# Optimization experiments

Hardware: AMD Instinct MI355X
Metric: run time of the kernel (lower is better)

## Reference

```python
import jax, jax.numpy as jnp
import numpy as np

S, P, T, E, H = 32, 48, 8, 64, 64      # scenes, peds/scene, obs_len, embedding_dim, h_dim
D1, D2 = 512, 1024                      # mlp_pre_pool hidden / bottleneck dims
B = S * P
TOTAL_LEN = 20                          # obs_len + pred_len (8 + 12)


def setup_inputs() -> dict:
    key = jax.random.key(0)
    ks = jax.random.split(key, 10)
    h_states = jax.random.normal(ks[0], (1, B, H), jnp.float32)
    end_pos = jax.random.normal(ks[1], (B, 2), jnp.float32)
    traj = jax.random.normal(ks[2], (TOTAL_LEN, B, 2), jnp.float32)
    traj_weight = jax.random.uniform(ks[3], (S, P * P, 2, T), jnp.float32)
    starts = jnp.arange(S, dtype=jnp.int32) * P
    seq_start_end = jnp.stack([starts, starts + P], axis=1)  # uniform scenes of P peds
    # learned params
    W_se = jax.random.normal(ks[4], (T * E, 2 * T), jnp.float32) * 0.05  # spatial_embedding
    b_se = jnp.zeros((T * E,), jnp.float32)
    W1 = jax.random.normal(ks[5], (D1, T * E + H), jnp.float32) * 0.05   # 576 -> 512
    b1 = jnp.zeros((D1,), jnp.float32)
    W2 = jax.random.normal(ks[6], (D2, D1), jnp.float32) * 0.05          # 512 -> 1024
    b2 = jnp.zeros((D2,), jnp.float32)
    return {"h_states": h_states, "seq_start_end": seq_start_end, "end_pos": end_pos,
            "traj": traj, "traj_weight": traj_weight, "mlp_pre_pool_dim_0": T * E,
            "W_se": W_se, "b_se": b_se, "W1": W1, "b1": b1, "W2": W2, "b2": b2}


def reference(h_states, seq_start_end, end_pos, traj, traj_weight, mlp_pre_pool_dim_0,
              W_se, b_se, W1, b1, W2, b2):
    # obs_traj: (obs_len, B, 2) -> (B, T, 2) -> per-scene (S, P, T, 2)
    obs = traj[:T].transpose(1, 0, 2).reshape(S, P, T, 2)
    h = h_states.reshape(S, P, H)
    # pairwise history differences: row (i, j) = obs[j] - obs[i]  (gather-diff)
    rel = obs[:, None, :, :, :] - obs[:, :, None, :, :]          # (S, i, j, T, 2)
    rel = rel.reshape(S, P, P, 2 * T)                            # flatten (T,2) -> 2T
    emb = rel @ W_se.T + b_se                                    # (S, P, P, T*E)
    # traj_weight[i]: (P*P, 2, T) -> permute(0,2,1) -> tile channel to E -> flatten
    w = jnp.transpose(traj_weight, (0, 1, 3, 2))                 # (S, P*P, T, 2)
    w = jnp.tile(w, (1, 1, 1, E // 2)).reshape(S, P, P, T * E)
    emb = w * emb
    # curr_hidden_1: hidden of ped j broadcast over i
    hj = jnp.broadcast_to(h[:, None, :, :], (S, P, P, H))
    x = jnp.concatenate([emb, hj], axis=-1)                      # (S, P, P, 576)
    x = jax.nn.relu(x @ W1.T + b1)                               # (S, P, P, 512)
    x = jax.nn.relu(x @ W2.T + b2)                               # (S, P, P, 1024)
    pool_h = x.max(axis=2)                                       # max over j
    return pool_h.reshape(S * P, D2)
```

## Files before the change

kernel.cpp:

```cpp
#include <hip/hip_runtime.h>
#include <hip/hip_bf16.h>
#include <stdint.h>

#define S_  32
#define P_  48
#define T_  8
#define E_  64
#define H_  64
#define D1_ 512
#define D2_ 1024
#define B_  (S_*P_)
#define M_  (S_*P_*P_)
#define K1_ 576
#define KE_ 512

typedef __attribute__((ext_vector_type(8))) short  short8;
typedef __attribute__((ext_vector_type(8))) __bf16 bf16x8;
typedef __attribute__((ext_vector_type(4))) float  f32x4;
typedef __attribute__((ext_vector_type(8))) float  f32x8;

__device__ inline short f2bf(float x) {
  union { float f; unsigned u; } v; v.f = x;
  unsigned r = v.u + 0x7FFFu + ((v.u >> 16) & 1u);
  return (short)(r >> 16);
}

__device__ inline void async16(const void* g, void* l) {
  __builtin_amdgcn_global_load_lds(
      (const __attribute__((address_space(1))) void*)g,
      (__attribute__((address_space(3))) void*)l, 16, 0, 0);
}

__device__ inline f32x4 mfma16(short8 a, short8 b, f32x4 c) {
  return __builtin_amdgcn_mfma_f32_16x16x32_bf16(
      __builtin_bit_cast(bf16x8, a), __builtin_bit_cast(bf16x8, b), c, 0, 0, 0);
}

__global__ __launch_bounds__(256) void k_cvt_w(const float* __restrict__ W1,
                                               const float* __restrict__ W2,
                                               short* __restrict__ W1b,
                                               short* __restrict__ W2b) {
  int idx = blockIdx.x * 256 + threadIdx.x;
  if (idx < D1_ * K1_) W1b[idx] = f2bf(W1[idx]);
  int idx2 = idx - D1_ * K1_;
  if (idx2 >= 0 && idx2 < D2_ * D1_) W2b[idx2] = f2bf(W2[idx2]);
}

__global__ __launch_bounds__(256) void k_oW(const float* __restrict__ traj,
                                            const float* __restrict__ Wse,
                                            float* __restrict__ oW) {
  int bid = blockIdx.x;
  int p = bid >> 1;
  int n = ((bid & 1) << 8) + threadIdx.x;
  float obs[16];
#pragma unroll
  for (int t = 0; t < T_; ++t) {
    obs[2*t]   = traj[(t*B_ + p)*2 + 0];
    obs[2*t+1] = traj[(t*B_ + p)*2 + 1];
  }
  float acc = 0.f;
#pragma unroll
  for (int k = 0; k < 16; ++k) acc += obs[k] * Wse[n*16 + k];
  oW[p*KE_ + n] = acc;
}

__global__ __launch_bounds__(256) void k_build_x(const float* __restrict__ tw,
                                                 const float* __restrict__ h,
                                                 const float* __restrict__ bse,
                                                 const float* __restrict__ oW,
                                                 short* __restrict__ X) {
  int tid = threadIdx.x;
  int wid = tid >> 6, lane = tid & 63;
  int row = blockIdx.x * 4 + wid;
  int s   = row / (P_ * P_);
  int rem = row - s * (P_ * P_);
  int i   = rem / P_;
  int j   = rem - i * P_;
  int bi = s * P_ + i, bj = s * P_ + j;

  const float* twq = tw + (size_t)(s * (P_*P_) + rem) * 16;
  int t = lane >> 3;
  float w0 = twq[t];
  float w1 = twq[8 + t];

  int n0 = lane * 8;
  f32x8 vj = *(const f32x8*)&oW[(size_t)bj * KE_ + n0];
  f32x8 vi = *(const f32x8*)&oW[(size_t)bi * KE_ + n0];
  f32x8 vb = *(const f32x8*)&bse[n0];
  short8 o;
#pragma unroll
  for (int k = 0; k < 8; ++k) {
    float e = (vj[k] - vi[k] + vb[k]) * ((k & 1) ? w1 : w0);
    o[k] = f2bf(e);
  }
  *(short8*)&X[(size_t)row * K1_ + n0] = o;

  if (lane < 8) {
    f32x8 vh = *(const f32x8*)&h[(size_t)bj * H_ + lane * 8];
    short8 oh;
#pragma unroll
    for (int k = 0; k < 8; ++k) oh[k] = f2bf(vh[k]);
    *(short8*)&X[(size_t)row * K1_ + KE_ + lane * 8] = oh;
  }
}

__global__ __launch_bounds__(256) void k_gemm1(const short* __restrict__ X,
                                               const short* __restrict__ W1b,
                                               const float* __restrict__ b1,
                                               short* __restrict__ X1) {
  __shared__ short Ae[128*64], Ao[128*64], Be[128*64], Bo[128*64];
  int tid = threadIdx.x;
  int wid = tid >> 6, lane = tid & 63;
  int wgid = (blockIdx.x & 7) * (2304/8) + (blockIdx.x >> 3);
  int tm = wgid >> 2, tn = wgid & 3;
  int brow = tm * 128, bcol = tn * 128;
  int wr = wid >> 1, wc = wid & 1;
  int lr = lane & 15, lhi = lane >> 4;
  int sx = lr & 7;

  f32x4 acc[4][4];
#pragma unroll
  for (int m = 0; m < 4; ++m)
#pragma unroll
    for (int n = 0; n < 4; ++n) acc[m][n] = (f32x4){0.f, 0.f, 0.f, 0.f};

  auto stage = [&](short* Ab, short* Bb, int k0) {
#pragma unroll
    for (int it = 0; it < 4; ++it) {
      int fg = it * 256 + tid;
      int r = fg >> 3, gs = (fg & 7) ^ (r & 7);
      async16(&X  [(size_t)(brow + r) * K1_ + k0 + (gs << 3)], &Ab[fg * 8]);
    }
#pragma unroll
    for (int it = 0; it < 4; ++it) {
      int fg = it * 256 + tid;
      int r = fg >> 3, gs = (fg & 7) ^ (r & 7);
      async16(&W1b[(size_t)(bcol + r) * K1_ + k0 + (gs << 3)], &Bb[fg * 8]);
    }
  };
  auto compute = [&](const short* Ab, const short* Bb) {
#pragma unroll
    for (int kk = 0; kk < 64; kk += 32) {
      int gr = (kk >> 3) + lhi;
      short8 a[4], b[4];
#pragma unroll
      for (int m = 0; m < 4; ++m)
        a[m] = *(const short8*)&Ab[(wr*64 + m*16 + lr) * 64 + ((gr ^ sx) << 3)];
#pragma unroll
      for (int n = 0; n < 4; ++n)
        b[n] = *(const short8*)&Bb[(wc*64 + n*16 + lr) * 64 + ((gr ^ sx) << 3)];
#pragma unroll
      for (int m = 0; m < 4; ++m)
#pragma unroll
        for (int n = 0; n < 4; ++n)
          acc[m][n] = mfma16(a[m], b[n], acc[m][n]);
    }
  };

  stage(Ae, Be, 0);
  __syncthreads();
  for (int ktp = 0; ktp < 4; ++ktp) {
    stage(Ao, Bo, ktp*128 + 64);
    compute(Ae, Be);
    __syncthreads();
    stage(Ae, Be, ktp*128 + 128);
    compute(Ao, Bo);
    __syncthreads();
  }
  compute(Ae, Be);

#pragma unroll
  for (int n = 0; n < 4; ++n) {
    int gcol = bcol + wc*64 + n*16 + lr;
    float bias = b1[gcol];
#pragma unroll
    for (int m = 0; m < 4; ++m) {
      int grow0 = brow + wr*64 + m*16 + lhi*4;
#pragma unroll
      for (int q = 0; q < 4; ++q) {
        float v = acc[m][n][q] + bias;
        v = v > 0.f ? v : 0.f;
        X1[(size_t)(grow0 + q) * D1_ + gcol] = f2bf(v);
      }
    }
  }
}

__global__ __launch_bounds__(256) void k_gemm2(const short* __restrict__ X1,
                                               const short* __restrict__ W2b,
                                               const float* __restrict__ b2,
                                               float* __restrict__ out) {
  __shared__ short Ae[96*64], Ao[96*64], Be[128*64], Bo[128*64];
  int tid = threadIdx.x;
  int wid = tid >> 6, lane = tid & 63;
  int wgid = (blockIdx.x & 7) * (6144/8) + (blockIdx.x >> 3);
  int tm = wgid >> 3, tn = wgid & 7;
  int brow = tm * 96, bcol = tn * 128;
  int wr = wid >> 1, wc = wid & 1;
  int lr = lane & 15, lhi = lane >> 4;
  int sx = lr & 7;

  f32x4 acc[3][4];
#pragma unroll
  for (int m = 0; m < 3; ++m)
#pragma unroll
    for (int n = 0; n < 4; ++n) acc[m][n] = (f32x4){0.f, 0.f, 0.f, 0.f};

  auto stage = [&](short* Ab, short* Bb, int k0) {
#pragma unroll
    for (int it = 0; it < 3; ++it) {
      int fg = it * 256 + tid;
      int r = fg >> 3, gs = (fg & 7) ^ (r & 7);
      async16(&X1 [(size_t)(brow + r) * D1_ + k0 + (gs << 3)], &Ab[fg * 8]);
    }
#pragma unroll
    for (int it = 0; it < 4; ++it) {
      int fg = it * 256 + tid;
      int r = fg >> 3, gs = (fg & 7) ^ (r & 7);
      async16(&W2b[(size_t)(bcol + r) * D1_ + k0 + (gs << 3)], &Bb[fg * 8]);
    }
  };
  auto compute = [&](const short* Ab, const short* Bb) {
#pragma unroll
    for (int kk = 0; kk < 64; kk += 32) {
      int gr = (kk >> 3) + lhi;
      short8 a[3], b[4];
#pragma unroll
      for (int m = 0; m < 3; ++m)
        a[m] = *(const short8*)&Ab[(wr*48 + m*16 + lr) * 64 + ((gr ^ sx) << 3)];
#pragma unroll
      for (int n = 0; n < 4; ++n)
        b[n] = *(const short8*)&Bb[(wc*64 + n*16 + lr) * 64 + ((gr ^ sx) << 3)];
#pragma unroll
      for (int m = 0; m < 3; ++m)
#pragma unroll
        for (int n = 0; n < 4; ++n)
          acc[m][n] = mfma16(a[m], b[n], acc[m][n]);
    }
  };

  stage(Ae, Be, 0);
  __syncthreads();
  for (int ktp = 0; ktp < 4; ++ktp) {
    stage(Ao, Bo, ktp*128 + 64);
    compute(Ae, Be);
    __syncthreads();
    if (ktp < 3) stage(Ae, Be, ktp*128 + 128);
    compute(Ao, Bo);
    __syncthreads();
  }

  int g = tm * 2 + wr;
#pragma unroll
  for (int n = 0; n < 4; ++n) {
    int gcol = bcol + wc*64 + n*16 + lr;
    float bias = b2[gcol];
    float r = 0.f;
#pragma unroll
    for (int m = 0; m < 3; ++m)
#pragma unroll
      for (int q = 0; q < 4; ++q) {
        float v = acc[m][n][q] + bias;
        if (v > r) r = v;
      }
    r = fmaxf(r, __shfl_xor(r, 16));
    r = fmaxf(r, __shfl_xor(r, 32));
    if (lhi == 0) out[(size_t)g * D2_ + gcol] = r;
  }
}

extern "C" void kernel_launch(void* const* d_in, const int* in_sizes, int n_in,
                              void* d_out, int out_size, void* d_ws, size_t ws_size,
                              hipStream_t stream) {
  const float* h_states = (const float*)d_in[0];
  const float* traj = (const float*)d_in[3];
  const float* tw   = (const float*)d_in[4];
  const float* Wse  = (const float*)d_in[6];
  const float* bse  = (const float*)d_in[7];
  const float* W1   = (const float*)d_in[8];
  const float* b1   = (const float*)d_in[9];
  const float* W2   = (const float*)d_in[10];
  const float* b2   = (const float*)d_in[11];
  float* out = (float*)d_out;

  char* ws = (char*)d_ws;
  const size_t X_BYTES   = (size_t)M_ * K1_ * 2;
  const size_t X1_BYTES  = (size_t)M_ * D1_ * 2;
  const size_t W1B_BYTES = (size_t)D1_ * K1_ * 2;
  short* X   = (short*)ws;
  short* X1  = (short*)(ws + X_BYTES);
  short* W1b = (short*)(ws + X_BYTES + X1_BYTES);
  short* W2b = (short*)(ws + X_BYTES + X1_BYTES + W1B_BYTES);
  float* oW  = (float*)(ws + X_BYTES);

  k_cvt_w  <<<(D1_*K1_ + D2_*D1_ + 255) / 256, 256, 0, stream>>>(W1, W2, W1b, W2b);
  k_oW     <<<B_ * 2, 256, 0, stream>>>(traj, Wse, oW);
  k_build_x<<<M_ / 4, 256, 0, stream>>>(tw, h_states, bse, oW, X);
  k_gemm1  <<<(M_ / 128) * (D1_ / 128), 256, 0, stream>>>(X, W1b, b1, X1);
  k_gemm2  <<<(M_ / 96) * (D2_ / 128), 256, 0, stream>>>(X1, W2b, b2, out);
}
```

Baseline: 255.2 us.

## Enlarge GEMM tiles to 256-wide with 8-wave blocks and MFMA priority hints

Both GEMMs move from 4-wave blocks with 128x128 (gemm1) and 96x128 (gemm2) tiles to 8-wave blocks with 256x256 and 192x256 tiles. Each wave now holds a larger accumulator set, which raises operand reuse per LDS load and cuts global traffic per FLOP. The K loop becomes a single double-buffered loop with explicit vmcnt waits and raw barriers, and MFMA bursts are wrapped in s_setprio. The gemm2 max-pool epilogue now reduces two scene-row groups per wave. The trade-off is fewer blocks (576 and 1536), which may leave CUs underused, plus higher register and LDS pressure that could lower occupancy.

```diff
diff --git a/kernel.cpp b/kernel.cpp
--- a/kernel.cpp
+++ b/kernel.cpp
@@ -104,78 +104,80 @@
   }
 }
 
-__global__ __launch_bounds__(256) void k_gemm1(const short* __restrict__ X,
-                                               const short* __restrict__ W1b,
-                                               const float* __restrict__ b1,
-                                               short* __restrict__ X1) {
-  __shared__ short Ae[128*64], Ao[128*64], Be[128*64], Bo[128*64];
+__global__ __launch_bounds__(512, 2) void k_gemm1(const short* __restrict__ X,
+                                                  const short* __restrict__ W1b,
+                                                  const float* __restrict__ b1,
+                                                  short* __restrict__ X1) {
+  __shared__ short Abuf[2][256 * 64];
+  __shared__ short Bbuf[2][256 * 64];
   int tid = threadIdx.x;
   int wid = tid >> 6, lane = tid & 63;
-  int wgid = (blockIdx.x & 7) * (2304/8) + (blockIdx.x >> 3);
-  int tm = wgid >> 2, tn = wgid & 3;
-  int brow = tm * 128, bcol = tn * 128;
-  int wr = wid >> 1, wc = wid & 1;
+  int wgid = (blockIdx.x & 7) * 72 + (blockIdx.x >> 3);
+  int tm = wgid >> 1, tn = wgid & 1;
+  int brow = tm * 256, bcol = tn * 256;
+  int wr = wid >> 2, wc = wid & 3;
   int lr = lane & 15, lhi = lane >> 4;
   int sx = lr & 7;
 
-  f32x4 acc[4][4];
-#pragma unroll
-  for (int m = 0; m < 4; ++m)
+  f32x4 acc[8][4];
+#pragma unroll
+  for (int m = 0; m < 8; ++m)
 #pragma unroll
     for (int n = 0; n < 4; ++n) acc[m][n] = (f32x4){0.f, 0.f, 0.f, 0.f};
 
-  auto stage = [&](short* Ab, short* Bb, int k0) {
+  auto stage = [&](int buf, int k0) {
 #pragma unroll
     for (int it = 0; it < 4; ++it) {
-      int fg = it * 256 + tid;
+      int fg = it * 512 + tid;
       int r = fg >> 3, gs = (fg & 7) ^ (r & 7);
-      async16(&X  [(size_t)(brow + r) * K1_ + k0 + (gs << 3)], &Ab[fg * 8]);
+      async16(&X  [(size_t)(brow + r) * K1_ + k0 + (gs << 3)], &Abuf[buf][fg * 8]);
     }
 #pragma unroll
     for (int it = 0; it < 4; ++it) {
-      int fg = it * 256 + tid;
+      int fg = it * 512 + tid;
       int r = fg >> 3, gs = (fg & 7) ^ (r & 7);
-      async16(&W1b[(size_t)(bcol + r) * K1_ + k0 + (gs << 3)], &Bb[fg * 8]);
+      async16(&W1b[(size_t)(bcol + r) * K1_ + k0 + (gs << 3)], &Bbuf[buf][fg * 8]);
     }
   };
-  auto compute = [&](const short* Ab, const short* Bb) {
-#pragma unroll
-    for (int kk = 0; kk < 64; kk += 32) {
-      int gr = (kk >> 3) + lhi;
-      short8 a[4], b[4];
-#pragma unroll
-      for (int m = 0; m < 4; ++m)
-        a[m] = *(const short8*)&Ab[(wr*64 + m*16 + lr) * 64 + ((gr ^ sx) << 3)];
+  auto compute = [&](int buf) {
+#pragma unroll
+    for (int kk = 0; kk < 2; ++kk) {
+      int gr = kk * 4 + lhi;
+      short8 a[8], b[4];
+#pragma unroll
+      for (int m = 0; m < 8; ++m)
+        a[m] = *(const short8*)&Abuf[buf][(wr*128 + m*16 + lr) * 64 + ((gr ^ sx) << 3)];
 #pragma unroll
       for (int n = 0; n < 4; ++n)
-        b[n] = *(const short8*)&Bb[(wc*64 + n*16 + lr) * 64 + ((gr ^ sx) << 3)];
-#pragma unroll
-      for (int m = 0; m < 4; ++m)
+        b[n] = *(const short8*)&Bbuf[buf][(wc*64 + n*16 + lr) * 64 + ((gr ^ sx) << 3)];
+      __builtin_amdgcn_s_setprio(1);
+#pragma unroll
+      for (int m = 0; m < 8; ++m)
 #pragma unroll
         for (int n = 0; n < 4; ++n)
           acc[m][n] = mfma16(a[m], b[n], acc[m][n]);
+      __builtin_amdgcn_s_setprio(0);
     }
   };
 
-  stage(Ae, Be, 0);
-  __syncthreads();
-  for (int ktp = 0; ktp < 4; ++ktp) {
-    stage(Ao, Bo, ktp*128 + 64);
-    compute(Ae, Be);
-    __syncthreads();
-    stage(Ae, Be, ktp*128 + 128);
-    compute(Ao, Bo);
-    __syncthreads();
-  }
-  compute(Ae, Be);
+  stage(0, 0);
+  asm volatile("s_waitcnt vmcnt(0)" ::: "memory");
+  __builtin_amdgcn_s_barrier();
+  for (int t = 0; t < 9; ++t) {
+    int cur = t & 1;
+    if (t + 1 < 9) stage(cur ^ 1, (t + 1) * 64);
+    compute(cur);
+    asm volatile("s_waitcnt vmcnt(0)" ::: "memory");
+    __builtin_amdgcn_s_barrier();
+  }
 
 #pragma unroll
   for (int n = 0; n < 4; ++n) {
     int gcol = bcol + wc*64 + n*16 + lr;
     float bias = b1[gcol];
 #pragma unroll
-    for (int m = 0; m < 4; ++m) {
-      int grow0 = brow + wr*64 + m*16 + lhi*4;
+    for (int m = 0; m < 8; ++m) {
+      int grow0 = brow + wr*128 + m*16 + lhi*4;
 #pragma unroll
       for (int q = 0; q < 4; ++q) {
         float v = acc[m][n][q] + bias;
@@ -186,86 +188,96 @@
   }
 }
 
-__global__ __launch_bounds__(256) void k_gemm2(const short* __restrict__ X1,
-                                               const short* __restrict__ W2b,
-                                               const float* __restrict__ b2,
-                                               float* __restrict__ out) {
-  __shared__ short Ae[96*64], Ao[96*64], Be[128*64], Bo[128*64];
+__global__ __launch_bounds__(512, 2) void k_gemm2(const short* __restrict__ X1,
+                                                  const short* __restrict__ W2b,
+                                                  const float* __restrict__ b2,
+                                                  float* __restrict__ out) {
+  __shared__ short Abuf[2][192 * 64];
+  __shared__ short Bbuf[2][256 * 64];
   int tid = threadIdx.x;
   int wid = tid >> 6, lane = tid & 63;
-  int wgid = (blockIdx.x & 7) * (6144/8) + (blockIdx.x >> 3);
-  int tm = wgid >> 3, tn = wgid & 7;
-  int brow = tm * 96, bcol = tn * 128;
-  int wr = wid >> 1, wc = wid & 1;
+  int wgid = (blockIdx.x & 7) * 192 + (blockIdx.x >> 3);
+  int tm = wgid >> 2, tn = wgid & 3;
+  int brow = tm * 192, bcol = tn * 256;
+  int wr = wid >> 2, wc = wid & 3;
   int lr = lane & 15, lhi = lane >> 4;
   int sx = lr & 7;
 
-  f32x4 acc[3][4];
-#pragma unroll
-  for (int m = 0; m < 3; ++m)
+  f32x4 acc[6][4];
+#pragma unroll
+  for (int m = 0; m < 6; ++m)
 #pragma unroll
     for (int n = 0; n < 4; ++n) acc[m][n] = (f32x4){0.f, 0.f, 0.f, 0.f};
 
-  auto stage = [&](short* Ab, short* Bb, int k0) {
+  auto stage = [&](int buf, int k0) {
 #pragma unroll
     for (int it = 0; it < 3; ++it) {
-      int fg = it * 256 + tid;
+      int fg = it * 512 + tid;
       int r = fg >> 3, gs = (fg & 7) ^ (r & 7);
-      async16(&X1 [(size_t)(brow + r) * D1_ + k0 + (gs << 3)], &Ab[fg * 8]);
+      async16(&X1 [(size_t)(brow + r) * D1_ + k0 + (gs << 3)], &Abuf[buf][fg * 8]);
     }
 #pragma unroll
     for (int it = 0; it < 4; ++it) {
-      int fg = it * 256 + tid;
+      int fg = it * 512 + tid;
       int r = fg >> 3, gs = (fg & 7) ^ (r & 7);
-      async16(&W2b[(size_t)(bcol + r) * D1_ + k0 + (gs << 3)], &Bb[fg * 8]);
+      async16(&W2b[(size_t)(bcol + r) * D1_ + k0 + (gs << 3)], &Bbuf[buf][fg * 8]);
     }
   };
-  auto compute = [&](const short* Ab, const short* Bb) {
-#pragma unroll
-    for (int kk = 0; kk < 64; kk += 32) {
-      int gr = (kk >> 3) + lhi;
-      short8 a[3], b[4];
-#pragma unroll
-      for (int m = 0; m < 3; ++m)
-        a[m] = *(const short8*)&Ab[(wr*48 + m*16 + lr) * 64 + ((gr ^ sx) << 3)];
+  auto compute = [&](int buf) {
+#pragma unroll
+    for (int kk = 0; kk < 2; ++kk) {
+      int gr = kk * 4 + lhi;
+      short8 a[6], b[4];
+#pragma unroll
+      for (int m = 0; m < 6; ++m)
+        a[m] = *(const short8*)&Abuf[buf][(wr*96 + m*16 + lr) * 64 + ((gr ^ sx) << 3)];
 #pragma unroll
       for (int n = 0; n < 4; ++n)
-        b[n] = *(const short8*)&Bb[(wc*64 + n*16 + lr) * 64 + ((gr ^ sx) << 3)];
-#pragma unroll
-      for (int m = 0; m < 3; ++m)
+        b[n] = *(const short8*)&Bbuf[buf][(wc*64 + n*16 + lr) * 64 + ((gr ^ sx) << 3)];
+      __builtin_amdgcn_s_setprio(1);
+#pragma unroll
+      for (int m = 0; m < 6; ++m)
 #pragma unroll
         for (int n = 0; n < 4; ++n)
           acc[m][n] = mfma16(a[m], b[n], acc[m][n]);
+      __builtin_amdgcn_s_setprio(0);
     }
   };
 
-  stage(Ae, Be, 0);
-  __syncthreads();
-  for (int ktp = 0; ktp < 4; ++ktp) {
-    stage(Ao, Bo, ktp*128 + 64);
-    compute(Ae, Be);
-    __syncthreads();
-    if (ktp < 3) stage(Ae, Be, ktp*128 + 128);
-    compute(Ao, Bo);
-    __syncthreads();
-  }
-
-  int g = tm * 2 + wr;
+  stage(0, 0);
+  asm volatile("s_waitcnt vmcnt(0)" ::: "memory");
+  __builtin_amdgcn_s_barrier();
+  for (int t = 0; t < 8; ++t) {
+    int cur = t & 1;
+    if (t + 1 < 8) stage(cur ^ 1, (t + 1) * 64);
+    compute(cur);
+    asm volatile("s_waitcnt vmcnt(0)" ::: "memory");
+    __builtin_amdgcn_s_barrier();
+  }
+
+  int gbase = tm * 4 + wr * 2;
 #pragma unroll
   for (int n = 0; n < 4; ++n) {
     int gcol = bcol + wc*64 + n*16 + lr;
     float bias = b2[gcol];
-    float r = 0.f;
+    float r0 = 0.f, r1 = 0.f;
 #pragma unroll
     for (int m = 0; m < 3; ++m)
 #pragma unroll
       for (int q = 0; q < 4; ++q) {
-        float v = acc[m][n][q] + bias;
-        if (v > r) r = v;
+        float v0 = acc[m][n][q] + bias;
+        float v1 = acc[m + 3][n][q] + bias;
+        if (v0 > r0) r0 = v0;
+        if (v1 > r1) r1 = v1;
       }
-    r = fmaxf(r, __shfl_xor(r, 16));
-    r = fmaxf(r, __shfl_xor(r, 32));
-    if (lhi == 0) out[(size_t)g * D2_ + gcol] = r;
+    r0 = fmaxf(r0, __shfl_xor(r0, 16));
+    r0 = fmaxf(r0, __shfl_xor(r0, 32));
+    r1 = fmaxf(r1, __shfl_xor(r1, 16));
+    r1 = fmaxf(r1, __shfl_xor(r1, 32));
+    if (lhi == 0) {
+      out[(size_t)gbase       * D2_ + gcol] = r0;
+      out[(size_t)(gbase + 1) * D2_ + gcol] = r1;
+    }
   }
 }
 
@@ -296,6 +308,6 @@
   k_cvt_w  <<<(D1_*K1_ + D2_*D1_ + 255) / 256, 256, 0, stream>>>(W1, W2, W1b, W2b);
   k_oW     <<<B_ * 2, 256, 0, stream>>>(traj, Wse, oW);
   k_build_x<<<M_ / 4, 256, 0, stream>>>(tw, h_states, bse, oW, X);
-  k_gemm1  <<<(M_ / 128) * (D1_ / 128), 256, 0, stream>>>(X, W1b, b1, X1);
-  k_gemm2  <<<(M_ / 96) * (D2_ / 128), 256, 0, stream>>>(X1, W2b, b2, out);
-}
+  k_gemm1  <<<(M_ / 256) * (D1_ / 256), 512, 0, stream>>>(X, W1b, b1, X1);
+  k_gemm2  <<<(M_ / 192) * (D2_ / 256), 512, 0, stream>>>(X1, W2b, b2, out);
+}
```

New measurement: 272.2 us. 1.07x slower.
